# Kernel optimization log

Hardware: AMD Instinct MI355X
Metric: run time of the kernel (lower is better)

## Reference

```python
import jax, jax.numpy as jnp
import numpy as np

N, E, DIN, DH, DP = 100000, 1600000, 128, 128, 64
BN_EPS = 1e-5


def setup_inputs() -> dict:
    key = jax.random.key(0)
    ks = jax.random.split(key, 24)

    def lin(k, fan_in, shape):
        return jax.random.normal(k, shape, jnp.float32) / np.sqrt(fan_in)

    inp = {
        "x": jax.random.normal(ks[0], (N, DIN), jnp.float32),
        "edge_index": jax.random.randint(ks[1], (2, E), 0, N, dtype=jnp.int32),
        "edge_type": jax.random.randint(ks[2], (E,), 0, 2, dtype=jnp.int32),
        "edge_weight": jax.random.uniform(ks[3], (E,), jnp.float32),
        "seed_node_id": 12345,
        # feature transform
        "ft_w": lin(ks[4], DIN, (DIN, DH)),
        "ft_b": jnp.zeros((DH,), jnp.float32),
        # GCN block 0: 2 layers, stacked along axis 0
        "g0_w": lin(ks[5], DH, (2, DH, DH)),
        "g0_b": jnp.zeros((2, DH), jnp.float32),
        "g0_gamma": jnp.ones((2, DH), jnp.float32),
        "g0_beta": jnp.zeros((2, DH), jnp.float32),
        "g0_rm": 0.1 * jax.random.normal(ks[6], (2, DH), jnp.float32),
        "g0_rv": 0.5 + jax.random.uniform(ks[7], (2, DH), jnp.float32),
        # GCN block 1
        "g1_w": lin(ks[8], DH, (2, DH, DH)),
        "g1_b": jnp.zeros((2, DH), jnp.float32),
        "g1_gamma": jnp.ones((2, DH), jnp.float32),
        "g1_beta": jnp.zeros((2, DH), jnp.float32),
        "g1_rm": 0.1 * jax.random.normal(ks[9], (2, DH), jnp.float32),
        "g1_rv": 0.5 + jax.random.uniform(ks[10], (2, DH), jnp.float32),
        # predictor (input = 4*DH)
        "p_w1": lin(ks[11], 4 * DH, (4 * DH, DP)),
        "p_b1": jnp.zeros((DP,), jnp.float32),
        "p_w2": lin(ks[12], DP, (DP, DP)),
        "p_b2": jnp.zeros((DP,), jnp.float32),
        "p_w3": lin(ks[13], DP, (DP, 1)),
        "p_b3": jnp.zeros((1,), jnp.float32),
    }
    return inp


def _gcn_conv(x, src, dst, w_e, W, b):
    # PyG GCNConv: linear transform, add self-loops (weight 1), symmetric norm, scatter-add, bias.
    h = x @ W                                               # [N, DH]
    deg = jax.ops.segment_sum(w_e, dst, num_segments=N) + 1.0
    dis = jax.lax.rsqrt(deg)
    coef = dis[src] * w_e * dis[dst]                        # [E]
    agg = jax.ops.segment_sum(coef[:, None] * h[src], dst, num_segments=N)
    return agg + h * (1.0 / deg)[:, None] + b               # self-loop norm = 1/deg


def _bn_eval(o, gamma, beta, rm, rv):
    return (o - rm) * gamma * jax.lax.rsqrt(rv + BN_EPS) + beta


def _gcn_block(x, src, dst, w_e, W, b, gamma, beta, rm, rv):
    # layer 0: no residual, followed by ReLU (dropout is a no-op in eval)
    h = _bn_eval(_gcn_conv(x, src, dst, w_e, W[0], b[0]), gamma[0], beta[0], rm[0], rv[0])
    h = jax.nn.relu(h)
    # layer 1: residual (in == out)
    h2 = _bn_eval(_gcn_conv(h, src, dst, w_e, W[1], b[1]), gamma[1], beta[1], rm[1], rv[1])
    return h2 + h


def reference(x, edge_index, edge_type, edge_weight, seed_node_id,
              ft_w, ft_b,
              g0_w, g0_b, g0_gamma, g0_beta, g0_rm, g0_rv,
              g1_w, g1_b, g1_gamma, g1_beta, g1_rm, g1_rv,
              p_w1, p_b1, p_w2, p_b2, p_w3, p_b3):
    src, dst = edge_index[0], edge_index[1]
    h = jax.nn.relu(x @ ft_w + ft_b)
    # edge-type masking via zeroed weights (identical math to slicing the edge list)
    w0 = edge_weight * (edge_type == 0).astype(edge_weight.dtype)
    w1 = edge_weight * (edge_type == 1).astype(edge_weight.dtype)
    x0 = _gcn_block(h, src, dst, w0, g0_w, g0_b, g0_gamma, g0_beta, g0_rm, g0_rv)
    x1 = _gcn_block(h, src, dst, w1, g1_w, g1_b, g1_gamma, g1_beta, g1_rm, g1_rv)
    s0 = jnp.broadcast_to(x0[seed_node_id], (N, DH))
    s1 = jnp.broadcast_to(x1[seed_node_id], (N, DH))
    xc = jnp.concatenate([x0, x1, s0, s1], axis=1)          # [N, 4*DH]
    z = jax.nn.relu(xc @ p_w1 + p_b1)
    z = jax.nn.relu(z @ p_w2 + p_b2)
    out = z @ p_w3 + p_b3                                   # [N, 1]
    return out.squeeze(-1)                                  # [N]
```

## Files before the change

### kernel.cpp

```cpp
#include <hip/hip_runtime.h>
#include <hip/hip_bf16.h>
#include <stdint.h>

#define N_NODES 100000

typedef unsigned short us16;
typedef short bf16x8 __attribute__((ext_vector_type(8)));
typedef float f32x4 __attribute__((ext_vector_type(4)));

__device__ __forceinline__ float us2f(us16 u){
  union{ unsigned int i; float f; } x; x.i = ((unsigned int)u) << 16; return x.f;
}
__device__ __forceinline__ us16 f2us(float f){
  union{ float f; unsigned int i; } x; x.f = f;
  unsigned int i = x.i;
  unsigned int r = (i + 0x7FFFu + ((i >> 16) & 1u)) >> 16;
  return (us16)r;
}

__global__ __launch_bounds__(256) void k_init(int* __restrict__ cnt, int n2){
  int i = blockIdx.x*256 + threadIdx.x;
  if (i < n2) cnt[i]=0;
}

__global__ __launch_bounds__(256) void k_scan_reduce(const int* __restrict__ in, int* __restrict__ bsum, int M){
  __shared__ int sd[256];
  int base = blockIdx.x*2048; int t = threadIdx.x;
  int sum = 0;
  #pragma unroll
  for(int i=0;i<8;i++){ int p = base + t*8 + i; if(p<M) sum += in[p]; }
  sd[t]=sum; __syncthreads();
  for(int s=128;s>0;s>>=1){ if(t<s) sd[t]+=sd[t+s]; __syncthreads(); }
  if(t==0) bsum[blockIdx.x]=sd[0];
}
__global__ void k_scan_top(int* __restrict__ bsum, int B){
  if (threadIdx.x==0){ int run=0; for(int i=0;i<B;i++){ int v=bsum[i]; bsum[i]=run; run+=v; } }
}
__global__ __launch_bounds__(256) void k_scan_apply(const int* __restrict__ in, const int* __restrict__ bsum,
                                                    int* __restrict__ out, int M){
  __shared__ int sd[256];
  int base = blockIdx.x*2048; int t = threadIdx.x;
  int loc[8]; int sum=0;
  #pragma unroll
  for(int i=0;i<8;i++){ int p = base + t*8 + i; int v = (p<M)?in[p]:0; loc[i]=sum; sum+=v; }
  sd[t]=sum; __syncthreads();
  for(int ofs=1;ofs<256;ofs<<=1){
    int v = (t>=ofs)? sd[t-ofs] : 0;
    __syncthreads();
    sd[t]+=v;
    __syncthreads();
  }
  int excl = ((t==0)?0:sd[t-1]) + bsum[blockIdx.x];
  #pragma unroll
  for(int i=0;i<8;i++){ int p = base + t*8 + i; if(p<M) out[p]=excl+loc[i]; }
}

__global__ __launch_bounds__(256) void k_deg_csr(const uint2* __restrict__ csr,
                                                 const int* __restrict__ rp, const int* __restrict__ cnt,
                                                 float* __restrict__ disA, int M){
  int i = blockIdx.x*256+threadIdx.x;
  if(i>=M) return;
  int e0 = rp[i], c = cnt[i];
  float s = 1.0f;
  for(int e=e0; e<e0+c; e++) s += __uint_as_float(csr[e].y);
  disA[i] = rsqrtf(s);
}

__global__ __launch_bounds__(256) void k_coef(uint2* __restrict__ csr,
                                              const int* __restrict__ rp,
                                              const float* __restrict__ disA, int E){
  int e = blockIdx.x*256+threadIdx.x;
  if(e>=E) return;
  int rpN = rp[N_NODES];
  int t = (e >= rpN) ? 1 : 0;
  uint2 q = csr[e];
  float w = __uint_as_float(q.y) * disA[t*N_NODES + (int)q.x];
  csr[e] = make_uint2(q.x, __float_as_uint(w));
}

__global__ __launch_bounds__(256) void k_prepw(const float* __restrict__ ft_w,
                                               const float* __restrict__ g0_w, const float* __restrict__ g1_w,
                                               const float* __restrict__ p_w1, const float* __restrict__ p_w2,
                                               us16* __restrict__ wt){
  int m = blockIdx.y;
  const float* srcp; int K, NCc; us16* dstp;
  switch(m){
    case 0: srcp=ft_w;        K=128; NCc=128; dstp=wt;        break;
    case 1: srcp=g0_w;        K=128; NCc=128; dstp=wt+16384;  break;
    case 2: srcp=g0_w+16384;  K=128; NCc=128; dstp=wt+32768;  break;
    case 3: srcp=g1_w;        K=128; NCc=128; dstp=wt+49152;  break;
    case 4: srcp=g1_w+16384;  K=128; NCc=128; dstp=wt+65536;  break;
    case 5: srcp=p_w1;        K=256; NCc=64;  dstp=wt+81920;  break;
    default:srcp=p_w2;        K=64;  NCc=64;  dstp=wt+98304;  break;
  }
  int idx = blockIdx.x*256+threadIdx.x;
  if(idx >= K*NCc) return;
  int nn = idx / K, k = idx - nn*K;
  dstp[idx] = f2us(srcp[(size_t)k*NCc + nn]);
}

template<int NC, typename AT>
__device__ __forceinline__ void mgemm_body(int bid,
                 const AT* __restrict__ A0, const AT* __restrict__ A1,
                 int lda, const us16* __restrict__ Wt,
                 const float* __restrict__ bias, const float* __restrict__ addv,
                 us16* __restrict__ C, int ldc, int n, int KC, int relu,
                 us16* Alds, us16* Wlds){
  constexpr int NB = NC/16;
  const int tid = threadIdx.x;
  const int lane = tid & 63, wid = tid >> 6;
  const int rowBase = bid*128;
  f32x4 zero = {0.f,0.f,0.f,0.f};
  f32x4 acc[2][NB];
  #pragma unroll
  for(int m=0;m<2;m++)
    #pragma unroll
    for(int nb=0;nb<NB;nb++) acc[m][nb] = zero;

  for(int kk=0; kk<KC; kk+=64){
    const AT* Ab = (kk<128)? A0 : A1;
    const int kc = (kk<128)? kk : (kk-128);
    #pragma unroll
    for(int p=0;p<4;p++){
      int idx = p*256 + tid;
      int r = idx>>3, u = idx&7;
      int row = rowBase + r;
      uint4 v = make_uint4(0u,0u,0u,0u);
      if(row<n){
        if constexpr (sizeof(AT)==2){
          v = *(const uint4*)(Ab + (size_t)row*lda + kc + u*8);
        } else {
          float4 f0 = *(const float4*)(Ab + (size_t)row*lda + kc + u*8);
          float4 f1 = *(const float4*)(Ab + (size_t)row*lda + kc + u*8 + 4);
          us16 tmp[8] = {f2us(f0.x),f2us(f0.y),f2us(f0.z),f2us(f0.w),
                         f2us(f1.x),f2us(f1.y),f2us(f1.z),f2us(f1.w)};
          v = *(const uint4*)tmp;
        }
      }
      *(uint4*)&Alds[(r*8 + (u ^ (r&7)))*8] = v;
    }
    #pragma unroll
    for(int p=0;p<NB/2;p++){
      int idx = p*256 + tid;
      int cI = idx>>3, u = idx&7;
      uint4 v = *(const uint4*)(Wt + (size_t)cI*KC + kk + u*8);
      *(uint4*)&Wlds[(cI*8 + (u ^ (cI&7)))*8] = v;
    }
    __syncthreads();
    #pragma unroll
    for(int ks=0;ks<2;ks++){
      bf16x8 af[2];
      #pragma unroll
      for(int m=0;m<2;m++){
        int r = wid*32 + m*16 + (lane&15);
        int u = (ks*4 + (lane>>4)) ^ (r&7);
        af[m] = *(const bf16x8*)&Alds[(r*8+u)*8];
      }
      #pragma unroll
      for(int nb=0;nb<NB;nb++){
        int c2 = nb*16 + (lane&15);
        int u = (ks*4 + (lane>>4)) ^ (c2&7);
        bf16x8 bfv = *(const bf16x8*)&Wlds[(c2*8+u)*8];
        #pragma unroll
        for(int m=0;m<2;m++)
          acc[m][nb] = __builtin_amdgcn_mfma_f32_16x16x32_bf16(af[m], bfv, acc[m][nb], 0,0,0);
      }
    }
    __syncthreads();
  }
  #pragma unroll
  for(int nb=0;nb<NB;nb++){
    int col = nb*16 + (lane&15);
    float badd = (bias? bias[col]:0.f) + (addv? addv[col]:0.f);
    #pragma unroll
    for(int m=0;m<2;m++){
      #pragma unroll
      for(int j=0;j<4;j++){
        int row = rowBase + wid*32 + m*16 + (lane>>4)*4 + j;
        if(row<n){
          float v = acc[m][nb][j] + badd;
          if(relu) v = fmaxf(v,0.f);
          C[(size_t)row*ldc + col] = f2us(v);
        }
      }
    }
  }
}

template<int NC, typename AT>
__global__ __launch_bounds__(256) void k_mgemm(const AT* __restrict__ A0, const AT* __restrict__ A1,
                 int lda, const us16* __restrict__ Wt,
                 const float* __restrict__ bias, const float* __restrict__ addv,
                 us16* __restrict__ C, int ldc, int n, int KC, int relu){
  __shared__ us16 smem[128*64 + NC*64];
  mgemm_body<NC,AT>(blockIdx.x, A0,A1,lda, Wt, bias,addv, C,ldc, n,KC,relu, smem, smem+128*64);
}

__global__ __launch_bounds__(256) void k_cnt_ft(const int* __restrict__ dst, const int* __restrict__ et,
    int* __restrict__ cnt, int* __restrict__ eofs, int E, int CB,
    const float* __restrict__ x, const us16* __restrict__ wt_ft, const float* __restrict__ ft_b,
    us16* __restrict__ B0, int n){
  __shared__ us16 smem[128*64 + 128*64];
  int b = blockIdx.x;
  if (b < CB){
    int e = b*256 + threadIdx.x;
    if (e < E){
      int d = dst[e]; int t = et[e];
      eofs[e] = atomicAdd(&cnt[t*N_NODES + d], 1);
    }
  } else {
    mgemm_body<128,float>(b - CB, x, x, 128, wt_ft, ft_b, nullptr, B0, 128, n, 128, 1,
                          smem, smem + 128*64);
  }
}

__global__ __launch_bounds__(256) void k_fill_l0(
    const int* __restrict__ src, const int* __restrict__ dst,
    const int* __restrict__ et, const float* __restrict__ ew,
    const int* __restrict__ rp, const int* __restrict__ eofs,
    uint2* __restrict__ csr, int E, int FB, int GB,
    const us16* __restrict__ B0,
    const us16* __restrict__ wt_g00, const us16* __restrict__ wt_g10,
    us16* __restrict__ B1, us16* __restrict__ B2, int n){
  __shared__ us16 smem[128*64 + 128*64];
  int b = blockIdx.x;
  if (b < FB){
    int e = b*256 + threadIdx.x;
    if (e < E){
      int s=src[e], d=dst[e], t=et[e]; float w=ew[e];
      int idx = t*N_NODES + d;
      int pos = rp[idx] + eofs[e];
      csr[pos] = make_uint2((unsigned)s, __float_as_uint(w));
    }
  } else if (b < FB + GB){
    mgemm_body<128,us16>(b - FB, B0, B0, 128, wt_g00, nullptr, nullptr, B1, 128, n, 128, 0,
                         smem, smem + 128*64);
  } else {
    mgemm_body<128,us16>(b - FB - GB, B0, B0, 128, wt_g10, nullptr, nullptr, B2, 128, n, 128, 0,
                         smem, smem + 128*64);
  }
}

__global__ __launch_bounds__(256) void k_agg(const us16* __restrict__ T,
  const uint2* __restrict__ csr,
  const int* __restrict__ rp, const int* __restrict__ cnt, int rowOfs,
  const float* __restrict__ dis,
  const float* __restrict__ bias, const float* __restrict__ gamma, const float* __restrict__ beta,
  const float* __restrict__ rm, const float* __restrict__ rv,
  const us16* __restrict__ resid,
  us16* __restrict__ out, int relu, int n){
  const int wid = threadIdx.x >> 6, lane = threadIdx.x & 63;
  const int hw = lane >> 5;
  const int sl = lane & 31;
  int r = blockIdx.x*8 + wid*2 + hw;
  if (r >= n) return;
  const int c0 = sl*4;
  int idx = rowOfs + r;
  int e0 = rp[idx];
  int ec = cnt[idx];
  const uint2* cp = csr + e0;
  float a0=0.f, a1=0.f, a2=0.f, a3=0.f;
  int nchunk = ec >> 2;
  int rem = ec & 3;
  for(int ch=0; ch<nchunk; ch++){
    uint2 q0 = cp[0], q1 = cp[1], q2 = cp[2], q3 = cp[3];
    cp += 4;
    uint2 va = *(const uint2*)(T + (size_t)q0.x*128 + c0);
    uint2 vb = *(const uint2*)(T + (size_t)q1.x*128 + c0);
    uint2 vc = *(const uint2*)(T + (size_t)q2.x*128 + c0);
    uint2 vd = *(const uint2*)(T + (size_t)q3.x*128 + c0);
    float ca = __uint_as_float(q0.y), cb = __uint_as_float(q1.y);
    float cc = __uint_as_float(q2.y), cd = __uint_as_float(q3.y);
    a0 += ca*us2f((us16)(va.x & 0xffffu));
    a1 += ca*us2f((us16)(va.x >> 16));
    a2 += ca*us2f((us16)(va.y & 0xffffu));
    a3 += ca*us2f((us16)(va.y >> 16));
    a0 += cb*us2f((us16)(vb.x & 0xffffu));
    a1 += cb*us2f((us16)(vb.x >> 16));
    a2 += cb*us2f((us16)(vb.y & 0xffffu));
    a3 += cb*us2f((us16)(vb.y >> 16));
    a0 += cc*us2f((us16)(vc.x & 0xffffu));
    a1 += cc*us2f((us16)(vc.x >> 16));
    a2 += cc*us2f((us16)(vc.y & 0xffffu));
    a3 += cc*us2f((us16)(vc.y >> 16));
    a0 += cd*us2f((us16)(vd.x & 0xffffu));
    a1 += cd*us2f((us16)(vd.x >> 16));
    a2 += cd*us2f((us16)(vd.y & 0xffffu));
    a3 += cd*us2f((us16)(vd.y >> 16));
  }
  for(int i=0;i<rem;i++){
    uint2 q = cp[i];
    float c = __uint_as_float(q.y);
    uint2 v = *(const uint2*)(T + (size_t)q.x*128 + c0);
    a0 += c*us2f((us16)(v.x & 0xffffu));
    a1 += c*us2f((us16)(v.x >> 16));
    a2 += c*us2f((us16)(v.y & 0xffffu));
    a3 += c*us2f((us16)(v.y >> 16));
  }
  float disr = dis[r]; float invdeg = disr*disr;
  uint2 vs = *(const uint2*)(T + (size_t)r*128 + c0);
  float4 bi = *(const float4*)(bias + c0);
  float4 ga = *(const float4*)(gamma + c0);
  float4 be = *(const float4*)(beta + c0);
  float4 rmv= *(const float4*)(rm + c0);
  float4 rvv= *(const float4*)(rv + c0);
  float o0 = a0*disr + us2f((us16)(vs.x & 0xffffu))*invdeg + bi.x;
  float o1 = a1*disr + us2f((us16)(vs.x >> 16))*invdeg + bi.y;
  float o2 = a2*disr + us2f((us16)(vs.y & 0xffffu))*invdeg + bi.z;
  float o3 = a3*disr + us2f((us16)(vs.y >> 16))*invdeg + bi.w;
  o0 = (o0 - rmv.x)*(ga.x*rsqrtf(rvv.x + 1e-5f)) + be.x;
  o1 = (o1 - rmv.y)*(ga.y*rsqrtf(rvv.y + 1e-5f)) + be.y;
  o2 = (o2 - rmv.z)*(ga.z*rsqrtf(rvv.z + 1e-5f)) + be.z;
  o3 = (o3 - rmv.w)*(ga.w*rsqrtf(rvv.w + 1e-5f)) + be.w;
  if (relu){
    o0=fmaxf(o0,0.f); o1=fmaxf(o1,0.f); o2=fmaxf(o2,0.f); o3=fmaxf(o3,0.f);
  }
  if (resid){
    uint2 vr = *(const uint2*)(resid + (size_t)r*128 + c0);
    o0 += us2f((us16)(vr.x & 0xffffu));
    o1 += us2f((us16)(vr.x >> 16));
    o2 += us2f((us16)(vr.y & 0xffffu));
    o3 += us2f((us16)(vr.y >> 16));
  }
  uint2 up;
  up.x = (unsigned)f2us(o0) | ((unsigned)f2us(o1) << 16);
  up.y = (unsigned)f2us(o2) | ((unsigned)f2us(o3) << 16);
  *(uint2*)(out + (size_t)r*128 + c0) = up;
}

__global__ void k_const64(const us16* __restrict__ X0, const us16* __restrict__ X1,
                          const int* __restrict__ seed,
                          const float* __restrict__ pw1, const float* __restrict__ pb1,
                          float* __restrict__ c64){
  int j = threadIdx.x;
  int s = seed[0];
  const us16* x0 = X0 + (size_t)s*128;
  const us16* x1 = X1 + (size_t)s*128;
  float acc = pb1[j];
  #pragma unroll 8
  for(int k=0;k<128;k++) acc += us2f(x0[k]) * pw1[(256+k)*64 + j];
  #pragma unroll 8
  for(int k=0;k<128;k++) acc += us2f(x1[k]) * pw1[(384+k)*64 + j];
  c64[j]=acc;
}

__global__ __launch_bounds__(256) void k_outdot(const us16* __restrict__ Z2, const float* __restrict__ w3,
                                                const float* __restrict__ b3, float* __restrict__ out, int n){
  int r = blockIdx.x*256 + threadIdx.x;
  if(r>=n) return;
  const us16* z = Z2 + (size_t)r*64;
  float acc = b3[0];
  #pragma unroll 8
  for(int j=0;j<64;j++) acc += us2f(z[j])*w3[j];
  out[r]=acc;
}

extern "C" void kernel_launch(void* const* d_in, const int* in_sizes, int n_in,
                              void* d_out, int out_size, void* d_ws, size_t ws_size,
                              hipStream_t stream){
  const int N = N_NODES;
  const int E = in_sizes[2];
  const float* x   = (const float*)d_in[0];
  const int*   ei  = (const int*)d_in[1];
  const int*   et  = (const int*)d_in[2];
  const float* ew  = (const float*)d_in[3];
  const int*   seed= (const int*)d_in[4];
  const float* ft_w= (const float*)d_in[5];
  const float* ft_b= (const float*)d_in[6];
  const float* g0_w= (const float*)d_in[7];
  const float* g0_b= (const float*)d_in[8];
  const float* g0_g= (const float*)d_in[9];
  const float* g0_be=(const float*)d_in[10];
  const float* g0_rm=(const float*)d_in[11];
  const float* g0_rv=(const float*)d_in[12];
  const float* g1_w= (const float*)d_in[13];
  const float* g1_b= (const float*)d_in[14];
  const float* g1_g= (const float*)d_in[15];
  const float* g1_be=(const float*)d_in[16];
  const float* g1_rm=(const float*)d_in[17];
  const float* g1_rv=(const float*)d_in[18];
  const float* p_w1= (const float*)d_in[19];
  const float* p_b1= (const float*)d_in[20];
  const float* p_w2= (const float*)d_in[21];
  const float* p_b2= (const float*)d_in[22];
  const float* p_w3= (const float*)d_in[23];
  const float* p_b3= (const float*)d_in[24];
  float* out = (float*)d_out;

  char* wsp = (char*)d_ws;
  auto alloc = [&](size_t bytes)->char*{ char* p = wsp; wsp += (bytes + 255) & ~(size_t)255; return p; };
  us16* B0 = (us16*)alloc((size_t)N*128*2);
  us16* B1 = (us16*)alloc((size_t)N*128*2);
  us16* B2 = (us16*)alloc((size_t)N*128*2);
  us16* B3 = (us16*)alloc((size_t)N*128*2);
  uint2* csr = (uint2*)alloc((size_t)E*8);
  float* disA=(float*)alloc((size_t)2*N*4);
  int* cnt =(int*)alloc((size_t)2*N*4);
  int* rp  =(int*)alloc((size_t)2*N*4);
  int* bsum=(int*)alloc(4096);
  float* c64=(float*)alloc(256);
  us16* wt =(us16*)alloc((size_t)102400*2);
  int* eofs = (int*)B3;
  us16* Z1 = B0;
  us16* Z2 = B1;

  const int* srcp = ei;
  const int* dstp = ei + E;

  int M = 2*N;
  int CB = (E+255)/256;
  int GB = (N+127)/128;
  int AB = (N+7)/8;
  int SB = (M+2047)/2048;

  k_init<<<(M+255)/256,256,0,stream>>>(cnt,M);
  dim3 pg(64,7);
  k_prepw<<<pg,256,0,stream>>>(ft_w,g0_w,g1_w,p_w1,p_w2,wt);

  const us16* wt_ft = wt;
  const us16* wt_g00= wt+16384;
  const us16* wt_g01= wt+32768;
  const us16* wt_g10= wt+49152;
  const us16* wt_g11= wt+65536;
  const us16* wt_p1 = wt+81920;
  const us16* wt_p2 = wt+98304;
  const float* dis0 = disA;
  const float* dis1 = disA + N;

  k_cnt_ft<<<CB+GB,256,0,stream>>>(dstp,et,cnt,eofs,E,CB, x,wt_ft,ft_b,B0,N);
  k_scan_reduce<<<SB,256,0,stream>>>(cnt,bsum,M);
  k_scan_top<<<1,64,0,stream>>>(bsum,SB);
  k_scan_apply<<<SB,256,0,stream>>>(cnt,bsum,rp,M);
  k_fill_l0<<<CB+2*GB,256,0,stream>>>(srcp,dstp,et,ew,rp,eofs,csr,E,CB,GB,
                                      B0,wt_g00,wt_g10,B1,B2,N);
  k_deg_csr<<<(M+255)/256,256,0,stream>>>(csr,rp,cnt,disA,M);
  k_coef<<<(E+255)/256,256,0,stream>>>(csr,rp,disA,E);

  k_agg<<<AB,256,0,stream>>>(B1,csr,rp,cnt,0,dis0,
                             g0_b,g0_g,g0_be,g0_rm,g0_rv, nullptr, B0,1,N);
  k_mgemm<128,us16><<<GB,256,0,stream>>>(B0,B0,128, wt_g01, nullptr,nullptr, B1,128, N,128,0);
  k_agg<<<AB,256,0,stream>>>(B1,csr,rp,cnt,0,dis0,
                             g0_b+128,g0_g+128,g0_be+128,g0_rm+128,g0_rv+128, B0, B3,0,N);
  k_agg<<<AB,256,0,stream>>>(B2,csr,rp,cnt,N,dis1,
                             g1_b,g1_g,g1_be,g1_rm,g1_rv, nullptr, B0,1,N);
  k_mgemm<128,us16><<<GB,256,0,stream>>>(B0,B0,128, wt_g11, nullptr,nullptr, B1,128, N,128,0);
  k_agg<<<AB,256,0,stream>>>(B1,csr,rp,cnt,N,dis1,
                             g1_b+128,g1_g+128,g1_be+128,g1_rm+128,g1_rv+128, B0, B2,0,N);
  k_const64<<<1,64,0,stream>>>(B3,B2,seed,p_w1,p_b1,c64);
  k_mgemm<64,us16><<<GB,256,0,stream>>>(B3,B2,128, wt_p1, nullptr, c64, Z1,64, N,256,1);
  k_mgemm<64,us16><<<GB,256,0,stream>>>(Z1,Z1,64,  wt_p2, p_b2, nullptr, Z2,64, N,64,1);
  k_outdot<<<(N+255)/256,256,0,stream>>>(Z2,p_w3,p_b3,out,N);
}
```

Baseline: 437.5 us.

## Batch both GCN blocks into combined aggregation and GEMM launches, regroup preprocessing

The two independent GCN blocks (edge type 0 and edge type 1) previously ran as four separate aggregation launches and two GEMM launches. They now run as two dual aggregation launches (k_agg2) and one dual GEMM launch (k_gemm2), each dispatching blocks for both graphs. Preprocessing is also regrouped: edge counting runs alone, the CSR fill shares a launch with the feature-transform GEMM, and the degree computation shares a launch with the first-layer GEMMs. The goal is fewer launches and fuller GPU occupancy per launch, with the serial scatter and degree phases overlapping GEMM work. In exchange, buffer aliasing gets more involved: B3 is reused after its eofs role, residuals are updated in place, and Z1/Z2 are packed into B1.

```diff
diff --git a/kernel.cpp b/kernel.cpp
--- a/kernel.cpp
+++ b/kernel.cpp
@@ -21,6 +21,16 @@
 __global__ __launch_bounds__(256) void k_init(int* __restrict__ cnt, int n2){
   int i = blockIdx.x*256 + threadIdx.x;
   if (i < n2) cnt[i]=0;
+}
+
+__global__ __launch_bounds__(256) void k_cnt(const int* __restrict__ dst,
+                                             const int* __restrict__ et,
+                                             int* __restrict__ cnt,
+                                             int* __restrict__ eofs, int E){
+  int e = blockIdx.x*256 + threadIdx.x;
+  if (e>=E) return;
+  int d = dst[e]; int t = et[e];
+  eofs[e] = atomicAdd(&cnt[t*N_NODES + d], 1);
 }
 
 __global__ __launch_bounds__(256) void k_scan_reduce(const int* __restrict__ in, int* __restrict__ bsum, int M){
@@ -53,17 +63,6 @@
   int excl = ((t==0)?0:sd[t-1]) + bsum[blockIdx.x];
   #pragma unroll
   for(int i=0;i<8;i++){ int p = base + t*8 + i; if(p<M) out[p]=excl+loc[i]; }
-}
-
-__global__ __launch_bounds__(256) void k_deg_csr(const uint2* __restrict__ csr,
-                                                 const int* __restrict__ rp, const int* __restrict__ cnt,
-                                                 float* __restrict__ disA, int M){
-  int i = blockIdx.x*256+threadIdx.x;
-  if(i>=M) return;
-  int e0 = rp[i], c = cnt[i];
-  float s = 1.0f;
-  for(int e=e0; e<e0+c; e++) s += __uint_as_float(csr[e].y);
-  disA[i] = rsqrtf(s);
 }
 
 __global__ __launch_bounds__(256) void k_coef(uint2* __restrict__ csr,
@@ -196,8 +195,11 @@
   mgemm_body<NC,AT>(blockIdx.x, A0,A1,lda, Wt, bias,addv, C,ldc, n,KC,relu, smem, smem+128*64);
 }
 
-__global__ __launch_bounds__(256) void k_cnt_ft(const int* __restrict__ dst, const int* __restrict__ et,
-    int* __restrict__ cnt, int* __restrict__ eofs, int E, int CB,
+__global__ __launch_bounds__(256) void k_fill_ft(
+    const int* __restrict__ src, const int* __restrict__ dst,
+    const int* __restrict__ et, const float* __restrict__ ew,
+    const int* __restrict__ rp, const int* __restrict__ eofs,
+    uint2* __restrict__ csr, int E, int CB,
     const float* __restrict__ x, const us16* __restrict__ wt_ft, const float* __restrict__ ft_b,
     us16* __restrict__ B0, int n){
   __shared__ us16 smem[128*64 + 128*64];
@@ -205,8 +207,10 @@
   if (b < CB){
     int e = b*256 + threadIdx.x;
     if (e < E){
-      int d = dst[e]; int t = et[e];
-      eofs[e] = atomicAdd(&cnt[t*N_NODES + d], 1);
+      int s=src[e], d=dst[e], t=et[e]; float w=ew[e];
+      int idx = t*N_NODES + d;
+      int pos = rp[idx] + eofs[e];
+      csr[pos] = make_uint2((unsigned)s, __float_as_uint(w));
     }
   } else {
     mgemm_body<128,float>(b - CB, x, x, 128, wt_ft, ft_b, nullptr, B0, 128, n, 128, 1,
@@ -214,34 +218,43 @@
   }
 }
 
-__global__ __launch_bounds__(256) void k_fill_l0(
-    const int* __restrict__ src, const int* __restrict__ dst,
-    const int* __restrict__ et, const float* __restrict__ ew,
-    const int* __restrict__ rp, const int* __restrict__ eofs,
-    uint2* __restrict__ csr, int E, int FB, int GB,
+__global__ __launch_bounds__(256) void k_deg_l0(
+    const uint2* __restrict__ csr, const int* __restrict__ rp, const int* __restrict__ cnt,
+    float* __restrict__ disA, int M, int DB, int GB,
     const us16* __restrict__ B0,
     const us16* __restrict__ wt_g00, const us16* __restrict__ wt_g10,
     us16* __restrict__ B1, us16* __restrict__ B2, int n){
   __shared__ us16 smem[128*64 + 128*64];
   int b = blockIdx.x;
-  if (b < FB){
-    int e = b*256 + threadIdx.x;
-    if (e < E){
-      int s=src[e], d=dst[e], t=et[e]; float w=ew[e];
-      int idx = t*N_NODES + d;
-      int pos = rp[idx] + eofs[e];
-      csr[pos] = make_uint2((unsigned)s, __float_as_uint(w));
-    }
-  } else if (b < FB + GB){
-    mgemm_body<128,us16>(b - FB, B0, B0, 128, wt_g00, nullptr, nullptr, B1, 128, n, 128, 0,
+  if (b < DB){
+    int i = b*256 + threadIdx.x;
+    if (i < M){
+      int e0 = rp[i], c = cnt[i];
+      float s = 1.0f;
+      for(int e=e0; e<e0+c; e++) s += __uint_as_float(csr[e].y);
+      disA[i] = rsqrtf(s);
+    }
+  } else if (b < DB + GB){
+    mgemm_body<128,us16>(b - DB, B0, B0, 128, wt_g00, nullptr, nullptr, B1, 128, n, 128, 0,
                          smem, smem + 128*64);
   } else {
-    mgemm_body<128,us16>(b - FB - GB, B0, B0, 128, wt_g10, nullptr, nullptr, B2, 128, n, 128, 0,
+    mgemm_body<128,us16>(b - DB - GB, B0, B0, 128, wt_g10, nullptr, nullptr, B2, 128, n, 128, 0,
                          smem, smem + 128*64);
   }
 }
 
-__global__ __launch_bounds__(256) void k_agg(const us16* __restrict__ T,
+__global__ __launch_bounds__(256) void k_gemm2(int GB,
+    const us16* __restrict__ Aa, const us16* __restrict__ Wa, us16* __restrict__ Ca,
+    const us16* __restrict__ Ab, const us16* __restrict__ Wb, us16* __restrict__ Cb, int n){
+  __shared__ us16 smem[128*64 + 128*64];
+  int b = blockIdx.x;
+  if (b < GB)
+    mgemm_body<128,us16>(b, Aa, Aa, 128, Wa, nullptr, nullptr, Ca, 128, n, 128, 0, smem, smem+128*64);
+  else
+    mgemm_body<128,us16>(b-GB, Ab, Ab, 128, Wb, nullptr, nullptr, Cb, 128, n, 128, 0, smem, smem+128*64);
+}
+
+__device__ __forceinline__ void agg_body(int bid, const us16* __restrict__ T,
   const uint2* __restrict__ csr,
   const int* __restrict__ rp, const int* __restrict__ cnt, int rowOfs,
   const float* __restrict__ dis,
@@ -252,7 +265,7 @@
   const int wid = threadIdx.x >> 6, lane = threadIdx.x & 63;
   const int hw = lane >> 5;
   const int sl = lane & 31;
-  int r = blockIdx.x*8 + wid*2 + hw;
+  int r = bid*8 + wid*2 + hw;
   if (r >= n) return;
   const int c0 = sl*4;
   int idx = rowOfs + r;
@@ -328,6 +341,24 @@
   *(uint2*)(out + (size_t)r*128 + c0) = up;
 }
 
+__global__ __launch_bounds__(256) void k_agg2(int AB,
+  const uint2* __restrict__ csr, const int* __restrict__ rp, const int* __restrict__ cnt,
+  const float* __restrict__ disA,
+  const us16* __restrict__ Ta,
+  const float* __restrict__ ba, const float* __restrict__ gaa, const float* __restrict__ bea,
+  const float* __restrict__ rma, const float* __restrict__ rva,
+  const us16* __restrict__ resida, us16* __restrict__ outa, int relua,
+  const us16* __restrict__ Tb,
+  const float* __restrict__ bb, const float* __restrict__ gab, const float* __restrict__ beb,
+  const float* __restrict__ rmb, const float* __restrict__ rvb,
+  const us16* __restrict__ residb, us16* __restrict__ outb, int relub, int n){
+  int b = blockIdx.x;
+  if (b < AB)
+    agg_body(b, Ta, csr, rp, cnt, 0, disA, ba,gaa,bea,rma,rva, resida, outa, relua, n);
+  else
+    agg_body(b-AB, Tb, csr, rp, cnt, N_NODES, disA+N_NODES, bb,gab,beb,rmb,rvb, residb, outb, relub, n);
+}
+
 __global__ void k_const64(const us16* __restrict__ X0, const us16* __restrict__ X1,
                           const int* __restrict__ seed,
                           const float* __restrict__ pw1, const float* __restrict__ pb1,
@@ -401,8 +432,8 @@
   float* c64=(float*)alloc(256);
   us16* wt =(us16*)alloc((size_t)102400*2);
   int* eofs = (int*)B3;
-  us16* Z1 = B0;
-  us16* Z2 = B1;
+  us16* Z1 = B1;
+  us16* Z2 = B1 + (size_t)N*64;
 
   const int* srcp = ei;
   const int* dstp = ei + E;
@@ -412,6 +443,7 @@
   int GB = (N+127)/128;
   int AB = (N+7)/8;
   int SB = (M+2047)/2048;
+  int DB = (M+255)/256;
 
   k_init<<<(M+255)/256,256,0,stream>>>(cnt,M);
   dim3 pg(64,7);
@@ -424,30 +456,25 @@
   const us16* wt_g11= wt+65536;
   const us16* wt_p1 = wt+81920;
   const us16* wt_p2 = wt+98304;
-  const float* dis0 = disA;
-  const float* dis1 = disA + N;
-
-  k_cnt_ft<<<CB+GB,256,0,stream>>>(dstp,et,cnt,eofs,E,CB, x,wt_ft,ft_b,B0,N);
+
+  k_cnt<<<CB,256,0,stream>>>(dstp,et,cnt,eofs,E);
   k_scan_reduce<<<SB,256,0,stream>>>(cnt,bsum,M);
   k_scan_top<<<1,64,0,stream>>>(bsum,SB);
   k_scan_apply<<<SB,256,0,stream>>>(cnt,bsum,rp,M);
-  k_fill_l0<<<CB+2*GB,256,0,stream>>>(srcp,dstp,et,ew,rp,eofs,csr,E,CB,GB,
-                                      B0,wt_g00,wt_g10,B1,B2,N);
-  k_deg_csr<<<(M+255)/256,256,0,stream>>>(csr,rp,cnt,disA,M);
+  k_fill_ft<<<CB+GB,256,0,stream>>>(srcp,dstp,et,ew,rp,eofs,csr,E,CB, x,wt_ft,ft_b,B0,N);
+  k_deg_l0<<<DB+2*GB,256,0,stream>>>(csr,rp,cnt,disA,M,DB,GB, B0,wt_g00,wt_g10,B1,B2,N);
   k_coef<<<(E+255)/256,256,0,stream>>>(csr,rp,disA,E);
 
-  k_agg<<<AB,256,0,stream>>>(B1,csr,rp,cnt,0,dis0,
-                             g0_b,g0_g,g0_be,g0_rm,g0_rv, nullptr, B0,1,N);
-  k_mgemm<128,us16><<<GB,256,0,stream>>>(B0,B0,128, wt_g01, nullptr,nullptr, B1,128, N,128,0);
-  k_agg<<<AB,256,0,stream>>>(B1,csr,rp,cnt,0,dis0,
-                             g0_b+128,g0_g+128,g0_be+128,g0_rm+128,g0_rv+128, B0, B3,0,N);
-  k_agg<<<AB,256,0,stream>>>(B2,csr,rp,cnt,N,dis1,
-                             g1_b,g1_g,g1_be,g1_rm,g1_rv, nullptr, B0,1,N);
-  k_mgemm<128,us16><<<GB,256,0,stream>>>(B0,B0,128, wt_g11, nullptr,nullptr, B1,128, N,128,0);
-  k_agg<<<AB,256,0,stream>>>(B1,csr,rp,cnt,N,dis1,
-                             g1_b+128,g1_g+128,g1_be+128,g1_rm+128,g1_rv+128, B0, B2,0,N);
-  k_const64<<<1,64,0,stream>>>(B3,B2,seed,p_w1,p_b1,c64);
-  k_mgemm<64,us16><<<GB,256,0,stream>>>(B3,B2,128, wt_p1, nullptr, c64, Z1,64, N,256,1);
+  k_agg2<<<2*AB,256,0,stream>>>(AB, csr,rp,cnt,disA,
+      B1, g0_b,g0_g,g0_be,g0_rm,g0_rv, nullptr, B0, 1,
+      B2, g1_b,g1_g,g1_be,g1_rm,g1_rv, nullptr, B3, 1, N);
+  k_gemm2<<<2*GB,256,0,stream>>>(GB, B0,wt_g01,B1, B3,wt_g11,B2, N);
+  k_agg2<<<2*AB,256,0,stream>>>(AB, csr,rp,cnt,disA,
+      B1, g0_b+128,g0_g+128,g0_be+128,g0_rm+128,g0_rv+128, B0, B0, 0,
+      B2, g1_b+128,g1_g+128,g1_be+128,g1_rm+128,g1_rv+128, B3, B3, 0, N);
+
+  k_const64<<<1,64,0,stream>>>(B0,B3,seed,p_w1,p_b1,c64);
+  k_mgemm<64,us16><<<GB,256,0,stream>>>(B0,B3,128, wt_p1, nullptr, c64, Z1,64, N,256,1);
   k_mgemm<64,us16><<<GB,256,0,stream>>>(Z1,Z1,64,  wt_p2, p_b2, nullptr, Z2,64, N,64,1);
   k_outdot<<<(N+255)/256,256,0,stream>>>(Z2,p_w3,p_b3,out,N);
 }
```

Measured after the change: 413.2 us. 1.06x faster.
